# Optimization experiments

Hardware: AMD Instinct MI355X
Metric: run time of the kernel (lower is better)

The kernel has to match this reference:

```python
import jax, jax.numpy as jnp
import numpy as np

THRESH = 0.7  # TWN-style threshold factor: delta = 0.7 * mean|W|


def ternarize(W):
    """Quantize latent float weights to alpha * {-1, 0, +1} (per-tensor scale)."""
    absW = jnp.abs(W)
    delta = THRESH * jnp.mean(absW)
    mask = (absW > delta).astype(W.dtype)
    n = jnp.maximum(jnp.sum(mask), 1.0)
    alpha = jnp.sum(absW * mask) / n
    return alpha * jnp.sign(W) * mask


def setup_inputs() -> dict:
    key = jax.random.key(0)
    k_x, k_w1, k_b1, k_w2, k_b2 = jax.random.split(key, 5)
    B = 65536
    x = jax.random.normal(k_x, (B, 784), dtype=jnp.float32)
    # latent float weights (torch Linear layout: [out, in]), kaiming-ish scale
    W1 = jax.random.normal(k_w1, (64, 784), dtype=jnp.float32) * (1.0 / np.sqrt(784))
    b1 = jax.random.normal(k_b1, (64,), dtype=jnp.float32) * 0.01
    W2 = jax.random.normal(k_w2, (10, 64), dtype=jnp.float32) * (1.0 / np.sqrt(64))
    b2 = jax.random.normal(k_b2, (10,), dtype=jnp.float32) * 0.01
    return {"x": x, "W1": W1, "b1": b1, "W2": W2, "b2": b2}


def reference(x, W1, b1, W2, b2):
    x = x.reshape(-1, 784)
    Wq1 = ternarize(W1)  # [64, 784]
    Wq2 = ternarize(W2)  # [10, 64]
    h = jax.nn.relu(x @ Wq1.T + b1)   # [B, 64]
    out = h @ Wq2.T + b2              # [B, 10]
    return out
```

## Files before the change

kernel.cpp:

```cpp
#include <hip/hip_runtime.h>
#include <hip/hip_bf16.h>


typedef __attribute__((ext_vector_type(4))) float f32x4;
typedef __attribute__((ext_vector_type(8))) short s16x8;

#define K1 784
#define K1_PAD 800
#define NHID 64
#define NOUT 10

static __device__ __forceinline__ unsigned short f2bf_rne(float f) {
    unsigned int u = __builtin_bit_cast(unsigned int, f);
    unsigned int r = u + 0x7FFFu + ((u >> 16) & 1u);
    return (unsigned short)(r >> 16);
}

static __device__ double block_sum(double v, double* red) {
    #pragma unroll
    for (int off = 32; off > 0; off >>= 1) v += __shfl_down(v, off, 64);
    const int w = threadIdx.x >> 6;
    const int lane = threadIdx.x & 63;
    __syncthreads();
    if (lane == 0) red[w] = v;
    __syncthreads();
    if (threadIdx.x == 0) {
        double t = 0.0;
        #pragma unroll
        for (int i = 0; i < 16; ++i) t += red[i];
        red[0] = t;
    }
    __syncthreads();
    return red[0];
}

__global__ __launch_bounds__(1024) void ternarize_kernel(
    const float* __restrict__ W1, const float* __restrict__ W2,
    unsigned short* __restrict__ W1q, unsigned short* __restrict__ W2q,
    float* __restrict__ alphas)
{
    __shared__ double red[16];
    const int tid = threadIdx.x;

    double s = 0.0;
    for (int i = tid; i < NHID * K1; i += 1024) s += (double)fabsf(W1[i]);
    s = block_sum(s, red);
    const float delta1 = (float)(0.7 * (s / (double)(NHID * K1)));

    double sm = 0.0, cn = 0.0;
    for (int i = tid; i < NHID * K1; i += 1024) {
        float a = fabsf(W1[i]);
        if (a > delta1) { sm += (double)a; cn += 1.0; }
    }
    sm = block_sum(sm, red);
    cn = block_sum(cn, red);
    const float alpha1 = (float)(sm / fmax(cn, 1.0));
    if (tid == 0) alphas[0] = alpha1;

    for (int i = tid; i < NHID * K1_PAD; i += 1024) {
        int n = i / K1_PAD;
        int k = i - n * K1_PAD;
        unsigned short v = 0;
        if (k < K1) {
            float w = W1[n * K1 + k];
            if (fabsf(w) > delta1) v = (w > 0.0f) ? 0x3F80u : 0xBF80u;
        }
        W1q[i] = v;
    }

    double s2 = 0.0;
    for (int i = tid; i < NOUT * NHID; i += 1024) s2 += (double)fabsf(W2[i]);
    s2 = block_sum(s2, red);
    const float delta2 = (float)(0.7 * (s2 / (double)(NOUT * NHID)));

    double sm2 = 0.0, cn2 = 0.0;
    for (int i = tid; i < NOUT * NHID; i += 1024) {
        float a = fabsf(W2[i]);
        if (a > delta2) { sm2 += (double)a; cn2 += 1.0; }
    }
    sm2 = block_sum(sm2, red);
    cn2 = block_sum(cn2, red);
    const float alpha2 = (float)(sm2 / fmax(cn2, 1.0));
    if (tid == 0) alphas[1] = alpha2;

    for (int i = tid; i < 16 * NHID; i += 1024) {
        int n = i >> 6;
        int k = i & 63;
        unsigned short v = 0;
        if (n < NOUT) {
            float w = W2[n * NHID + k];
            if (fabsf(w) > delta2) v = (w > 0.0f) ? 0x3F80u : 0xBF80u;
        }
        W2q[i] = v;
    }
}

__global__ __launch_bounds__(256) void fused_kernel(
    const float* __restrict__ x,
    const float* __restrict__ b1,
    const float* __restrict__ b2,
    const short* __restrict__ W1q,
    const short* __restrict__ W2q,
    const float* __restrict__ alphas,
    float* __restrict__ out)
{
    const int tid  = threadIdx.x;
    const int wave = tid >> 6;
    const int lane = tid & 63;
    const int low  = lane & 15;
    const int quad = lane >> 4;

    const int m0 = blockIdx.x * 64 + wave * 16;
    const float* xrow = x + (size_t)(m0 + low) * K1;

    f32x4 acc[4];
    #pragma unroll
    for (int nt = 0; nt < 4; ++nt) acc[nt] = (f32x4){0.f, 0.f, 0.f, 0.f};

    for (int ks = 0; ks < 25; ++ks) {
        const int kf = ks * 32 + quad * 8;
        s16x8 a;
        if (kf + 8 <= K1) {
            f32x4 p = *(const f32x4*)(xrow + kf);
            f32x4 q = *(const f32x4*)(xrow + kf + 4);
            a[0] = (short)f2bf_rne(p[0]); a[1] = (short)f2bf_rne(p[1]);
            a[2] = (short)f2bf_rne(p[2]); a[3] = (short)f2bf_rne(p[3]);
            a[4] = (short)f2bf_rne(q[0]); a[5] = (short)f2bf_rne(q[1]);
            a[6] = (short)f2bf_rne(q[2]); a[7] = (short)f2bf_rne(q[3]);
        } else {
            a = (s16x8)(short)0;
        }
        s16x8 b[4];
        #pragma unroll
        for (int nt = 0; nt < 4; ++nt)
            b[nt] = *(const s16x8*)(W1q + (size_t)(nt * 16 + low) * K1_PAD + kf);
        #pragma unroll
        for (int nt = 0; nt < 4; ++nt)
            acc[nt] = __builtin_amdgcn_mfma_f32_16x16x32_bf16(a, b[nt], acc[nt], 0, 0, 0);
    }

    const float alpha1 = alphas[0];
    const float alpha2 = alphas[1];

    __shared__ __align__(16) unsigned short h_lds[4][16][72];
    #pragma unroll
    for (int nt = 0; nt < 4; ++nt) {
        const int n = nt * 16 + low;
        const float bias = b1[n];
        #pragma unroll
        for (int r = 0; r < 4; ++r) {
            float hv = fmaxf(0.0f, fmaf(alpha1, acc[nt][r], bias));
            h_lds[wave][quad * 4 + r][n] = f2bf_rne(hv);
        }
    }
    __syncthreads();

    s16x8 a0 = *(const s16x8*)(&h_lds[wave][low][quad * 8]);
    s16x8 a1 = *(const s16x8*)(&h_lds[wave][low][32 + quad * 8]);
    s16x8 w0 = *(const s16x8*)(W2q + low * 64 + quad * 8);
    s16x8 w1 = *(const s16x8*)(W2q + low * 64 + 32 + quad * 8);

    f32x4 acc2 = (f32x4){0.f, 0.f, 0.f, 0.f};
    acc2 = __builtin_amdgcn_mfma_f32_16x16x32_bf16(a0, w0, acc2, 0, 0, 0);
    acc2 = __builtin_amdgcn_mfma_f32_16x16x32_bf16(a1, w1, acc2, 0, 0, 0);

    if (low < NOUT) {
        const float bias2 = b2[low];
        #pragma unroll
        for (int r = 0; r < 4; ++r) {
            const int row = m0 + quad * 4 + r;
            out[(size_t)row * NOUT + low] = fmaf(alpha2, acc2[r], bias2);
        }
    }
}

extern "C" void kernel_launch(void* const* d_in, const int* in_sizes, int n_in,
                              void* d_out, int out_size, void* d_ws, size_t ws_size,
                              hipStream_t stream) {
    const float* x  = (const float*)d_in[0];
    const float* W1 = (const float*)d_in[1];
    const float* b1 = (const float*)d_in[2];
    const float* W2 = (const float*)d_in[3];
    const float* b2 = (const float*)d_in[4];
    float* out = (float*)d_out;

    const int nrows = in_sizes[0] / K1;

    unsigned short* W1q = (unsigned short*)d_ws;
    unsigned short* W2q = W1q + NHID * K1_PAD;
    float* alphas = (float*)(W2q + 16 * NHID);

    ternarize_kernel<<<1, 1024, 0, stream>>>(W1, W2, W1q, W2q, alphas);

    const int nblocks = nrows / 64;
    fused_kernel<<<nblocks, 256, 0, stream>>>(x, b1, b2, (const short*)W1q,
                                              (const short*)W2q, alphas, out);
}
```

Baseline: 346.4 us.

## Parallelize ternarization across blocks and stage x tiles through LDS with prefetch

The single-block 1024-thread ternarize kernel is split into two multi-block kernels (sum, then quantize with fused alpha accumulation) that combine per-block partials with double atomics into a zeroed header. The fused GEMM kernel now loads x with coalesced row-contiguous float4 loads, converts to bf16, and stages them through double-buffered LDS, prefetching the next k-slice. The block-wide barrier is replaced by a per-wave waitcnt. This targets the serial latency of the one-block ternarize launch and uncoalesced x loads, at the cost of an extra memset and kernel launch and more LDS traffic. The double-atomic summation order is also nondeterministic.

```diff
diff --git a/kernel.cpp b/kernel.cpp
--- a/kernel.cpp
+++ b/kernel.cpp
@@ -4,6 +4,7 @@
 
 typedef __attribute__((ext_vector_type(4))) float f32x4;
 typedef __attribute__((ext_vector_type(8))) short s16x8;
+typedef __attribute__((ext_vector_type(4))) short s16x4;
 
 #define K1 784
 #define K1_PAD 800
@@ -16,7 +17,7 @@
     return (unsigned short)(r >> 16);
 }
 
-static __device__ double block_sum(double v, double* red) {
+static __device__ double block_sum256(double v, double* red) {
     #pragma unroll
     for (int off = 32; off > 0; off >>= 1) v += __shfl_down(v, off, 64);
     const int w = threadIdx.x >> 6;
@@ -24,74 +25,70 @@
     __syncthreads();
     if (lane == 0) red[w] = v;
     __syncthreads();
-    if (threadIdx.x == 0) {
-        double t = 0.0;
-        #pragma unroll
-        for (int i = 0; i < 16; ++i) t += red[i];
-        red[0] = t;
-    }
-    __syncthreads();
-    return red[0];
-}
-
-__global__ __launch_bounds__(1024) void ternarize_kernel(
+    return red[0] + red[1] + red[2] + red[3];
+}
+
+__global__ __launch_bounds__(256) void tern_sum_kernel(
+    const float* __restrict__ W1, const float* __restrict__ W2,
+    double* __restrict__ hdr)
+{
+    __shared__ double red[4];
+    double s = 0.0;
+    for (int i = blockIdx.x * 256 + threadIdx.x; i < NHID * K1; i += gridDim.x * 256)
+        s += (double)fabsf(W1[i]);
+    s = block_sum256(s, red);
+    if (threadIdx.x == 0) atomicAdd(&hdr[0], s);
+
+    if (blockIdx.x == 0) {
+        double s2 = 0.0;
+        for (int i = threadIdx.x; i < NOUT * NHID; i += 256)
+            s2 += (double)fabsf(W2[i]);
+        s2 = block_sum256(s2, red);
+        if (threadIdx.x == 0) atomicAdd(&hdr[1], s2);
+    }
+}
+
+__global__ __launch_bounds__(256) void tern_quant_kernel(
     const float* __restrict__ W1, const float* __restrict__ W2,
     unsigned short* __restrict__ W1q, unsigned short* __restrict__ W2q,
-    float* __restrict__ alphas)
+    double* __restrict__ hdr)
 {
-    __shared__ double red[16];
-    const int tid = threadIdx.x;
-
-    double s = 0.0;
-    for (int i = tid; i < NHID * K1; i += 1024) s += (double)fabsf(W1[i]);
-    s = block_sum(s, red);
-    const float delta1 = (float)(0.7 * (s / (double)(NHID * K1)));
+    __shared__ double red[4];
+    const float delta1 = (float)(0.7 * hdr[0] / (double)(NHID * K1));
 
     double sm = 0.0, cn = 0.0;
-    for (int i = tid; i < NHID * K1; i += 1024) {
-        float a = fabsf(W1[i]);
-        if (a > delta1) { sm += (double)a; cn += 1.0; }
-    }
-    sm = block_sum(sm, red);
-    cn = block_sum(cn, red);
-    const float alpha1 = (float)(sm / fmax(cn, 1.0));
-    if (tid == 0) alphas[0] = alpha1;
-
-    for (int i = tid; i < NHID * K1_PAD; i += 1024) {
+    for (int i = blockIdx.x * 256 + threadIdx.x; i < NHID * K1_PAD; i += gridDim.x * 256) {
         int n = i / K1_PAD;
         int k = i - n * K1_PAD;
         unsigned short v = 0;
         if (k < K1) {
             float w = W1[n * K1 + k];
-            if (fabsf(w) > delta1) v = (w > 0.0f) ? 0x3F80u : 0xBF80u;
+            float a = fabsf(w);
+            if (a > delta1) { v = (w > 0.0f) ? 0x3F80u : 0xBF80u; sm += (double)a; cn += 1.0; }
         }
         W1q[i] = v;
     }
-
-    double s2 = 0.0;
-    for (int i = tid; i < NOUT * NHID; i += 1024) s2 += (double)fabsf(W2[i]);
-    s2 = block_sum(s2, red);
-    const float delta2 = (float)(0.7 * (s2 / (double)(NOUT * NHID)));
-
-    double sm2 = 0.0, cn2 = 0.0;
-    for (int i = tid; i < NOUT * NHID; i += 1024) {
-        float a = fabsf(W2[i]);
-        if (a > delta2) { sm2 += (double)a; cn2 += 1.0; }
-    }
-    sm2 = block_sum(sm2, red);
-    cn2 = block_sum(cn2, red);
-    const float alpha2 = (float)(sm2 / fmax(cn2, 1.0));
-    if (tid == 0) alphas[1] = alpha2;
-
-    for (int i = tid; i < 16 * NHID; i += 1024) {
-        int n = i >> 6;
-        int k = i & 63;
-        unsigned short v = 0;
-        if (n < NOUT) {
-            float w = W2[n * NHID + k];
-            if (fabsf(w) > delta2) v = (w > 0.0f) ? 0x3F80u : 0xBF80u;
-        }
-        W2q[i] = v;
+    sm = block_sum256(sm, red);
+    cn = block_sum256(cn, red);
+    if (threadIdx.x == 0) { atomicAdd(&hdr[2], sm); atomicAdd(&hdr[3], cn); }
+
+    if (blockIdx.x == 0) {
+        const float delta2 = (float)(0.7 * hdr[1] / (double)(NOUT * NHID));
+        double sm2 = 0.0, cn2 = 0.0;
+        for (int i = threadIdx.x; i < 16 * NHID; i += 256) {
+            int n = i >> 6;
+            int k = i & 63;
+            unsigned short v = 0;
+            if (n < NOUT) {
+                float w = W2[n * NHID + k];
+                float a = fabsf(w);
+                if (a > delta2) { v = (w > 0.0f) ? 0x3F80u : 0xBF80u; sm2 += (double)a; cn2 += 1.0; }
+            }
+            W2q[i] = v;
+        }
+        sm2 = block_sum256(sm2, red);
+        cn2 = block_sum256(cn2, red);
+        if (threadIdx.x == 0) { atomicAdd(&hdr[4], sm2); atomicAdd(&hdr[5], cn2); }
     }
 }
 
@@ -101,7 +98,7 @@
     const float* __restrict__ b2,
     const short* __restrict__ W1q,
     const short* __restrict__ W2q,
-    const float* __restrict__ alphas,
+    const double* __restrict__ hdr,
     float* __restrict__ out)
 {
     const int tid  = threadIdx.x;
@@ -111,38 +108,61 @@
     const int quad = lane >> 4;
 
     const int m0 = blockIdx.x * 64 + wave * 16;
-    const float* xrow = x + (size_t)(m0 + low) * K1;
+
+    const int srow = lane >> 3;
+    const int scol = lane & 7;
+    const float* g0 = x + (size_t)(m0 + srow) * K1 + scol * 4;
+    const float* g1 = x + (size_t)(m0 + 8 + srow) * K1 + scol * 4;
+
+    __shared__ __align__(16) unsigned short stage[4][2][16][32];
+    __shared__ __align__(16) unsigned short h_lds[4][16][72];
+
+    const short* wbase = W1q + (size_t)low * K1_PAD + quad * 8;
 
     f32x4 acc[4];
     #pragma unroll
     for (int nt = 0; nt < 4; ++nt) acc[nt] = (f32x4){0.f, 0.f, 0.f, 0.f};
 
+    const f32x4 zero4 = (f32x4){0.f, 0.f, 0.f, 0.f};
+
+    f32x4 c0 = *(const f32x4*)(g0);
+    f32x4 c1 = *(const f32x4*)(g1);
+
+    int buf = 0;
     for (int ks = 0; ks < 25; ++ks) {
-        const int kf = ks * 32 + quad * 8;
-        s16x8 a;
-        if (kf + 8 <= K1) {
-            f32x4 p = *(const f32x4*)(xrow + kf);
-            f32x4 q = *(const f32x4*)(xrow + kf + 4);
-            a[0] = (short)f2bf_rne(p[0]); a[1] = (short)f2bf_rne(p[1]);
-            a[2] = (short)f2bf_rne(p[2]); a[3] = (short)f2bf_rne(p[3]);
-            a[4] = (short)f2bf_rne(q[0]); a[5] = (short)f2bf_rne(q[1]);
-            a[6] = (short)f2bf_rne(q[2]); a[7] = (short)f2bf_rne(q[3]);
-        } else {
-            a = (s16x8)(short)0;
-        }
-        s16x8 b[4];
+        f32x4 n0 = zero4, n1 = zero4;
+        if (ks < 24) {
+            const int kf = (ks + 1) * 32 + scol * 4;
+            if (kf < K1) {
+                n0 = *(const f32x4*)(g0 + (ks + 1) * 32);
+                n1 = *(const f32x4*)(g1 + (ks + 1) * 32);
+            }
+        }
+
+        s16x4 p0, p1;
+        p0[0] = (short)f2bf_rne(c0[0]); p0[1] = (short)f2bf_rne(c0[1]);
+        p0[2] = (short)f2bf_rne(c0[2]); p0[3] = (short)f2bf_rne(c0[3]);
+        p1[0] = (short)f2bf_rne(c1[0]); p1[1] = (short)f2bf_rne(c1[1]);
+        p1[2] = (short)f2bf_rne(c1[2]); p1[3] = (short)f2bf_rne(c1[3]);
+        *(s16x4*)&stage[wave][buf][srow][scol * 4]     = p0;
+        *(s16x4*)&stage[wave][buf][8 + srow][scol * 4] = p1;
+
+        __asm__ volatile("s_waitcnt lgkmcnt(0)" ::: "memory");
+
+        s16x8 a = *(const s16x8*)&stage[wave][buf][low][quad * 8];
+        const short* wk = wbase + ks * 32;
         #pragma unroll
-        for (int nt = 0; nt < 4; ++nt)
-            b[nt] = *(const s16x8*)(W1q + (size_t)(nt * 16 + low) * K1_PAD + kf);
-        #pragma unroll
-        for (int nt = 0; nt < 4; ++nt)
-            acc[nt] = __builtin_amdgcn_mfma_f32_16x16x32_bf16(a, b[nt], acc[nt], 0, 0, 0);
-    }
-
-    const float alpha1 = alphas[0];
-    const float alpha2 = alphas[1];
-
-    __shared__ __align__(16) unsigned short h_lds[4][16][72];
+        for (int nt = 0; nt < 4; ++nt) {
+            s16x8 b = *(const s16x8*)(wk + (size_t)nt * 16 * K1_PAD);
+            acc[nt] = __builtin_amdgcn_mfma_f32_16x16x32_bf16(a, b, acc[nt], 0, 0, 0);
+        }
+
+        c0 = n0; c1 = n1; buf ^= 1;
+    }
+
+    const float alpha1 = (float)(hdr[2] / fmax(hdr[3], 1.0));
+    const float alpha2 = (float)(hdr[4] / fmax(hdr[5], 1.0));
+
     #pragma unroll
     for (int nt = 0; nt < 4; ++nt) {
         const int n = nt * 16 + low;
@@ -153,7 +173,7 @@
             h_lds[wave][quad * 4 + r][n] = f2bf_rne(hv);
         }
     }
-    __syncthreads();
+    __asm__ volatile("s_waitcnt lgkmcnt(0)" ::: "memory");
 
     s16x8 a0 = *(const s16x8*)(&h_lds[wave][low][quad * 8]);
     s16x8 a1 = *(const s16x8*)(&h_lds[wave][low][32 + quad * 8]);
@@ -186,13 +206,16 @@
 
     const int nrows = in_sizes[0] / K1;
 
-    unsigned short* W1q = (unsigned short*)d_ws;
+    double* hdr = (double*)d_ws;
+    unsigned short* W1q = (unsigned short*)((char*)d_ws + 64);
     unsigned short* W2q = W1q + NHID * K1_PAD;
-    float* alphas = (float*)(W2q + 16 * NHID);
-
-    ternarize_kernel<<<1, 1024, 0, stream>>>(W1, W2, W1q, W2q, alphas);
+
+    hipMemsetAsync(d_ws, 0, 64, stream);
+
+    tern_sum_kernel<<<64, 256, 0, stream>>>(W1, W2, hdr);
+    tern_quant_kernel<<<64, 256, 0, stream>>>(W1, W2, W1q, W2q, hdr);
 
     const int nblocks = nrows / 64;
     fused_kernel<<<nblocks, 256, 0, stream>>>(x, b1, b2, (const short*)W1q,
-                                              (const short*)W2q, alphas, out);
-}
+                                              (const short*)W2q, hdr, out);
+}
```

Result: faster. 307.6 us, median of 2 (-11.2%).
